# Optimization experiments

Measured on AMD Instinct MI355X. Metric: run time of the kernel, lower is better.

## Reference

```python
import jax, jax.numpy as jnp
import numpy as np

SIZE_IN = 1024
SIZE_OUT = 1024
N_ROWS = 16384
MAX_VAL = 127.0  # nemo=False -> int8 path


def _quantize(t, max_val):
    """Per-tensor symmetric quantization matching the torch code.
    scale = max_val / max(|min(t)|, |max(t)|) (1.0 if t_max==0);
    q = clamp(round(scale*t), -max_val, max_val) cast to int8."""
    t_max = jnp.maximum(jnp.abs(jnp.min(t)), jnp.abs(jnp.max(t)))
    t_max = jnp.where(t_max == 0.0, 1.0, t_max)
    scale = max_val / t_max
    q = jnp.clip(jnp.round(scale * t), -max_val, max_val).astype(jnp.int8)
    return q, scale


def setup_inputs() -> dict:
    key = jax.random.key(0)
    kx, kw, kb = jax.random.split(key, 3)
    x = jax.random.normal(kx, (N_ROWS, SIZE_IN), dtype=jnp.float32)
    # kaiming_uniform_(a=sqrt(5)) -> uniform(-1/sqrt(fan_in), 1/sqrt(fan_in))
    bound = 1.0 / np.sqrt(SIZE_IN)
    weight = jax.random.uniform(kw, (SIZE_OUT, SIZE_IN), dtype=jnp.float32,
                                minval=-bound, maxval=bound)
    bias = jax.random.uniform(kb, (SIZE_OUT,), dtype=jnp.float32,
                              minval=-bound, maxval=bound)
    return {"x": x, "weight": weight, "bias": bias}


def reference(x, weight, bias):
    qw, sw = _quantize(weight, MAX_VAL)          # [SIZE_OUT, SIZE_IN] int8
    qx, sa = _quantize(x, MAX_VAL)               # [N, SIZE_IN] int8
    qb, sb = _quantize(bias, MAX_VAL)            # [SIZE_OUT] int8
    # for the approximate axx kernel), then dequantize.
    acc = jnp.matmul(qx.astype(jnp.int32), qw.astype(jnp.int32).T)  # [N, SIZE_OUT]
    out = acc.astype(jnp.float32) / (sa * sw)
    out = out + qb.astype(jnp.float32) / sb
    return out
```

## Files before the change

### kernel.cpp

```cpp
#include <hip/hip_runtime.h>


#define M_ROWS 16384
#define K_DIM  1024
#define N_OUT  1024

typedef int v4i __attribute__((ext_vector_type(4)));

__device__ __forceinline__ void gload_lds16(const void* g, void* l) {
  __builtin_amdgcn_global_load_lds(
      (const __attribute__((address_space(1))) void*)g,
      (__attribute__((address_space(3))) void*)l, 16, 0, 0);
}

__device__ __forceinline__ float block_reduce_max4(float m, float* red) {
#pragma unroll
  for (int off = 32; off > 0; off >>= 1)
    m = fmaxf(m, __shfl_down(m, off));
  const int wid = threadIdx.x >> 6, lane = threadIdx.x & 63;
  if (lane == 0) red[wid] = m;
  __syncthreads();
  float r = fmaxf(fmaxf(red[0], red[1]), fmaxf(red[2], red[3]));
  __syncthreads();
  return r;
}

__global__ void amax_stage1(const float* __restrict__ src, int n4,
                            float* __restrict__ partials) {
  __shared__ float red[4];
  float m = 0.0f;
  const int stride = gridDim.x * blockDim.x;
  for (int idx = blockIdx.x * blockDim.x + threadIdx.x; idx < n4; idx += stride) {
    float4 v = ((const float4*)src)[idx];
    m = fmaxf(m, fmaxf(fmaxf(fabsf(v.x), fabsf(v.y)), fmaxf(fabsf(v.z), fabsf(v.w))));
  }
  float r = block_reduce_max4(m, red);
  if (threadIdx.x == 0) partials[blockIdx.x] = r;
}

__global__ void finalize_kernel(const float* __restrict__ px, int npx,
                                const float* __restrict__ pw, int npw,
                                const float* __restrict__ bias,
                                float* __restrict__ amax,
                                float* __restrict__ bdeq) {
  __shared__ float red[4];
  const int tid = threadIdx.x;

  float m = 0.0f;
  for (int i = tid; i < npx; i += 256) m = fmaxf(m, px[i]);
  float rx = block_reduce_max4(m, red);

  m = 0.0f;
  for (int i = tid; i < npw; i += 256) m = fmaxf(m, pw[i]);
  float rw = block_reduce_max4(m, red);

  float4 bv = ((const float4*)bias)[tid];
  m = fmaxf(fmaxf(fabsf(bv.x), fabsf(bv.y)), fmaxf(fabsf(bv.z), fabsf(bv.w)));
  float rb = block_reduce_max4(m, red);

  if (rx == 0.0f) rx = 1.0f;
  if (rw == 0.0f) rw = 1.0f;
  if (rb == 0.0f) rb = 1.0f;
  if (tid == 0) {
    amax[0] = rx;
    amax[1] = rw;
    amax[2] = rb;
  }
  const float sb = 127.0f / rb;
  float4 q;
  q.x = fminf(fmaxf(rintf(sb * bv.x), -127.0f), 127.0f) / sb;
  q.y = fminf(fmaxf(rintf(sb * bv.y), -127.0f), 127.0f) / sb;
  q.z = fminf(fmaxf(rintf(sb * bv.z), -127.0f), 127.0f) / sb;
  q.w = fminf(fmaxf(rintf(sb * bv.w), -127.0f), 127.0f) / sb;
  ((float4*)bdeq)[tid] = q;
}

__global__ void quant_kernel(const float* __restrict__ src, signed char* __restrict__ dst,
                             int n4, const float* __restrict__ amax, int slot) {
  const float s = 127.0f / amax[slot];
  const int stride = gridDim.x * blockDim.x;
  for (int idx = blockIdx.x * blockDim.x + threadIdx.x; idx < n4; idx += stride) {
    float4 v = ((const float4*)src)[idx];
    int q0 = (int)fminf(fmaxf(rintf(s * v.x), -127.0f), 127.0f);
    int q1 = (int)fminf(fmaxf(rintf(s * v.y), -127.0f), 127.0f);
    int q2 = (int)fminf(fmaxf(rintf(s * v.z), -127.0f), 127.0f);
    int q3 = (int)fminf(fmaxf(rintf(s * v.w), -127.0f), 127.0f);
    unsigned int packed = (q0 & 0xff) | ((q1 & 0xff) << 8) |
                          ((q2 & 0xff) << 16) | ((q3 & 0xff) << 24);
    ((unsigned int*)dst)[idx] = packed;
  }
}


__global__ __launch_bounds__(512, 2) void gemm_kernel(
    const signed char* __restrict__ qx, const signed char* __restrict__ qw,
    const float* __restrict__ amax, const float* __restrict__ bdeq,
    float* __restrict__ out) {
  __shared__ char lds[131072];

  const int tid  = threadIdx.x;
  const int w    = tid >> 6;
  const int lane = tid & 63;
  const int wm = w >> 2;
  const int wn = w & 3;
  const int fr = lane & 15;
  const int q  = lane >> 4;

  const int bid = blockIdx.x;
  const int wg  = (bid & 7) * 32 + (bid >> 3);
  const int Mbase = (wg >> 2) * 256;
  const int Nbase = (wg & 3) * 256;

  const signed char* gA = qx + (size_t)Mbase * K_DIM;
  const signed char* gB = qw + (size_t)Nbase * K_DIM;

  const int lrow = lane >> 3;
  const int lcol = ((lane & 7) ^ lrow) << 4;

  const int u0    = (q ^ (fr & 7)) << 4;
  const int aoffA = (wm * 64 + fr) * 128 + u0;
  const int aoffB = (wn * 32 + fr) * 128 + u0;

  v4i acc[8][4] = {};
  v4i Ar[4][2];
  v4i Br[2][2][2];

#define STG(MAT, BUF, HALF, T)                                                 \
  do {                                                                         \
    const signed char* _gb = (MAT) ? gB : gA;                                  \
    char* _l = lds + ((MAT) ? 65536 : 0) + (BUF)*32768 + (HALF)*16384 +        \
               w * 2048;                                                       \
    size_t _ro = (size_t)((HALF)*128 + w * 16 + lrow) * K_DIM + (T)*128 + lcol;\
    gload_lds16(_gb + _ro, _l);                                                \
    gload_lds16(_gb + _ro + (size_t)8 * K_DIM, _l + 1024);                     \
  } while (0)

#define RD_A(BUF, MH)                                                          \
  do {                                                                         \
    const char* _A = lds + (BUF)*32768 + (MH)*16384;                           \
    _Pragma("unroll") for (int f = 0; f < 4; ++f) {                            \
      Ar[f][0] = *(const v4i*)(_A + (aoffA + f * 2048));                       \
      Ar[f][1] = *(const v4i*)(_A + ((aoffA ^ 64) + f * 2048));                \
    }                                                                          \
  } while (0)

#define RD_B(BUF, NH)                                                          \
  do {                                                                         \
    const char* _B = lds + 65536 + (BUF)*32768 + (NH)*16384;                   \
    _Pragma("unroll") for (int g = 0; g < 2; ++g) {                            \
      Br[NH][g][0] = *(const v4i*)(_B + (aoffB + g * 2048));                   \
      Br[NH][g][1] = *(const v4i*)(_B + ((aoffB ^ 64) + g * 2048));            \
    }                                                                          \
  } while (0)

#define MM(MH, NH)                                                             \
  do {                                                                         \
    __builtin_amdgcn_s_barrier();                                              \
    asm volatile("s_waitcnt lgkmcnt(0)" ::: "memory");                         \
    __builtin_amdgcn_sched_barrier(0);                                         \
    __builtin_amdgcn_s_setprio(1);                                             \
    _Pragma("unroll") for (int kk = 0; kk < 2; ++kk)                           \
      _Pragma("unroll") for (int f = 0; f < 4; ++f)                            \
        _Pragma("unroll") for (int g = 0; g < 2; ++g)                          \
          acc[(MH)*4 + f][(NH)*2 + g] = __builtin_amdgcn_mfma_i32_16x16x64_i8( \
              Ar[f][kk], Br[NH][g][kk], acc[(MH)*4 + f][(NH)*2 + g], 0, 0, 0); \
    __builtin_amdgcn_s_setprio(0);                                             \
  } while (0)

#define VM(N) asm volatile("s_waitcnt vmcnt(" #N ")" ::: "memory")
#define BAR() __builtin_amdgcn_s_barrier()

  STG(0, 0, 0, 0); STG(1, 0, 0, 0); STG(1, 0, 1, 0); STG(0, 0, 1, 0);
  STG(0, 1, 0, 1); STG(1, 1, 0, 1); STG(1, 1, 1, 1); STG(0, 1, 1, 1);
  VM(8);
  BAR();

  for (int j = 0; j < 4; ++j) {
    const int t2 = (2 * j + 2) & 7;
    const int t3 = (2 * j + 3) & 7;
    RD_A(0, 0); RD_B(0, 0);                    MM(0, 0);        BAR();
    RD_B(0, 1); STG(0, 0, 0, t2);              MM(0, 1);        BAR();
    RD_A(0, 1); STG(1, 0, 0, t2);              MM(1, 1);        BAR();
    STG(1, 0, 1, t2);                          MM(1, 0); VM(6); BAR();
    RD_A(1, 0); RD_B(1, 0); STG(0, 0, 1, t2);  MM(0, 0);        BAR();
    RD_B(1, 1); STG(0, 1, 0, t3); STG(1, 1, 0, t3); MM(0, 1);   BAR();
    RD_A(1, 1); STG(1, 1, 1, t3);              MM(1, 1);        BAR();
    STG(0, 1, 1, t3);                          MM(1, 0); VM(8); BAR();
  }
#undef MM
#undef RD_A
#undef RD_B
#undef STG
#undef VM
#undef BAR

  const float inv_denom = (amax[0] * amax[1]) * (1.0f / 16129.0f);
#pragma unroll
  for (int f = 0; f < 8; ++f) {
    const int row0 = Mbase + wm * 64 + (f & 3) * 16 + (f >> 2) * 128 + q * 4;
#pragma unroll
    for (int g = 0; g < 4; ++g) {
      const int col = Nbase + wn * 32 + (g & 1) * 16 + (g >> 1) * 128 + fr;
      const float bb = bdeq[col];
#pragma unroll
      for (int i = 0; i < 4; ++i) {
        out[(size_t)(row0 + i) * N_OUT + col] = (float)acc[f][g][i] * inv_denom + bb;
      }
    }
  }
}

extern "C" void kernel_launch(void* const* d_in, const int* in_sizes, int n_in,
                              void* d_out, int out_size, void* d_ws, size_t ws_size,
                              hipStream_t stream) {
  const float* x = (const float*)d_in[0];
  const float* w = (const float*)d_in[1];
  const float* b = (const float*)d_in[2];
  float* out = (float*)d_out;

  char* ws = (char*)d_ws;
  float* amax = (float*)ws;
  float* bdeq = (float*)(ws + 256);
  float* px   = (float*)(ws + 8192);
  float* pw   = (float*)(ws + 16384 + 8192);
  signed char* qw = (signed char*)(ws + 65536);
  signed char* qx = (signed char*)(ws + (1 << 21));

  const int NPX = 2048, NPW = 256;
  hipLaunchKernelGGL(amax_stage1, dim3(NPX), dim3(256), 0, stream, x, M_ROWS * K_DIM / 4, px);
  hipLaunchKernelGGL(amax_stage1, dim3(NPW), dim3(256), 0, stream, w, N_OUT * K_DIM / 4, pw);
  hipLaunchKernelGGL(finalize_kernel, dim3(1), dim3(256), 0, stream, px, NPX, pw, NPW, b, amax, bdeq);
  hipLaunchKernelGGL(quant_kernel, dim3(2048), dim3(256), 0, stream, x, qx, M_ROWS * K_DIM / 4, amax, 0);
  hipLaunchKernelGGL(quant_kernel, dim3(256), dim3(256), 0, stream, w, qw, N_OUT * K_DIM / 4, amax, 1);
  hipLaunchKernelGGL(gemm_kernel, dim3(64 * 4), dim3(512), 0, stream, qx, qw, amax, bdeq, out);
}
```

Before: 65.62 us.

## Peel last K iteration, interleave epilogue stores with final MFMAs, drop extra barrier

```diff
diff --git a/kernel.cpp b/kernel.cpp
--- a/kernel.cpp
+++ b/kernel.cpp
@@ -121,6 +121,8 @@
   const int aoffA = (wm * 64 + fr) * 128 + u0;
   const int aoffB = (wn * 32 + fr) * 128 + u0;
 
+  const float inv_denom = (amax[0] * amax[1]) * (1.0f / 16129.0f);
+
   v4i acc[8][4] = {};
   v4i Ar[4][2];
   v4i Br[2][2][2];
@@ -153,61 +155,70 @@
     }                                                                          \
   } while (0)
 
-#define MM(MH, NH)                                                             \
-  do {                                                                         \
-    __builtin_amdgcn_s_barrier();                                              \
-    asm volatile("s_waitcnt lgkmcnt(0)" ::: "memory");                         \
-    __builtin_amdgcn_sched_barrier(0);                                         \
-    __builtin_amdgcn_s_setprio(1);                                             \
+#define MFMA_Q(MH, NH)                                                         \
+  do {                                                                         \
     _Pragma("unroll") for (int kk = 0; kk < 2; ++kk)                           \
       _Pragma("unroll") for (int f = 0; f < 4; ++f)                            \
         _Pragma("unroll") for (int g = 0; g < 2; ++g)                          \
           acc[(MH)*4 + f][(NH)*2 + g] = __builtin_amdgcn_mfma_i32_16x16x64_i8( \
               Ar[f][kk], Br[NH][g][kk], acc[(MH)*4 + f][(NH)*2 + g], 0, 0, 0); \
-    __builtin_amdgcn_s_setprio(0);                                             \
+  } while (0)
+
+#define STORE_Q(MH, NH)                                                        \
+  do {                                                                         \
+    _Pragma("unroll") for (int f = 0; f < 4; ++f) {                            \
+      const int _row0 = Mbase + wm * 64 + f * 16 + (MH)*128 + q * 4;           \
+      _Pragma("unroll") for (int g = 0; g < 2; ++g) {                          \
+        const int _col = Nbase + wn * 32 + g * 16 + (NH)*128 + fr;             \
+        const float _bb = bdeq[_col];                                          \
+        _Pragma("unroll") for (int i = 0; i < 4; ++i)                          \
+          out[(size_t)(_row0 + i) * N_OUT + _col] =                            \
+              (float)acc[(MH)*4 + f][(NH)*2 + g][i] * inv_denom + _bb;         \
+      }                                                                        \
+    }                                                                          \
   } while (0)
 
 #define VM(N) asm volatile("s_waitcnt vmcnt(" #N ")" ::: "memory")
-#define BAR() __builtin_amdgcn_s_barrier()
+#define ENDPH()                                                                \
+  do {                                                                         \
+    asm volatile("s_waitcnt lgkmcnt(0)" ::: "memory");                         \
+    __builtin_amdgcn_s_barrier();                                              \
+  } while (0)
 
   STG(0, 0, 0, 0); STG(1, 0, 0, 0); STG(1, 0, 1, 0); STG(0, 0, 1, 0);
   STG(0, 1, 0, 1); STG(1, 1, 0, 1); STG(1, 1, 1, 1); STG(0, 1, 1, 1);
   VM(8);
-  BAR();
-
-  for (int j = 0; j < 4; ++j) {
-    const int t2 = (2 * j + 2) & 7;
-    const int t3 = (2 * j + 3) & 7;
-    RD_A(0, 0); RD_B(0, 0);                    MM(0, 0);        BAR();
-    RD_B(0, 1); STG(0, 0, 0, t2);              MM(0, 1);        BAR();
-    RD_A(0, 1); STG(1, 0, 0, t2);              MM(1, 1);        BAR();
-    STG(1, 0, 1, t2);                          MM(1, 0); VM(6); BAR();
-    RD_A(1, 0); RD_B(1, 0); STG(0, 0, 1, t2);  MM(0, 0);        BAR();
-    RD_B(1, 1); STG(0, 1, 0, t3); STG(1, 1, 0, t3); MM(0, 1);   BAR();
-    RD_A(1, 1); STG(1, 1, 1, t3);              MM(1, 1);        BAR();
-    STG(0, 1, 1, t3);                          MM(1, 0); VM(8); BAR();
-  }
-#undef MM
+  __builtin_amdgcn_s_barrier();
+
+  for (int j = 0; j < 3; ++j) {
+    const int t2 = 2 * j + 2;
+    const int t3 = 2 * j + 3;
+    RD_A(0, 0); RD_B(0, 0);                    MFMA_Q(0, 0);        ENDPH();
+    STG(0, 0, 0, t2); RD_B(0, 1);              MFMA_Q(0, 1);        ENDPH();
+    STG(1, 0, 0, t2); RD_A(0, 1);              MFMA_Q(1, 1);        ENDPH();
+    STG(1, 0, 1, t2);                          MFMA_Q(1, 0); VM(6); ENDPH();
+    STG(0, 0, 1, t2); RD_A(1, 0); RD_B(1, 0);  MFMA_Q(0, 0);        ENDPH();
+    STG(0, 1, 0, t3); STG(1, 1, 0, t3); RD_B(1, 1); MFMA_Q(0, 1);   ENDPH();
+    STG(1, 1, 1, t3); RD_A(1, 1);              MFMA_Q(1, 1);        ENDPH();
+    STG(0, 1, 1, t3);                          MFMA_Q(1, 0); VM(8); ENDPH();
+  }
+
+  RD_A(0, 0); RD_B(0, 0);  MFMA_Q(0, 0);        ENDPH();
+  RD_B(0, 1);              MFMA_Q(0, 1);        ENDPH();
+  RD_A(0, 1);              MFMA_Q(1, 1);        ENDPH();
+                           MFMA_Q(1, 0); VM(0); ENDPH();
+  RD_A(1, 0); RD_B(1, 0);  MFMA_Q(0, 0);  STORE_Q(0, 0);
+  RD_B(1, 1);              MFMA_Q(0, 1);  STORE_Q(0, 1);
+  RD_A(1, 1);              MFMA_Q(1, 1);  STORE_Q(1, 1);
+                           MFMA_Q(1, 0);  STORE_Q(1, 0);
+
+#undef STG
 #undef RD_A
 #undef RD_B
-#undef STG
+#undef MFMA_Q
+#undef STORE_Q
 #undef VM
-#undef BAR
-
-  const float inv_denom = (amax[0] * amax[1]) * (1.0f / 16129.0f);
-#pragma unroll
-  for (int f = 0; f < 8; ++f) {
-    const int row0 = Mbase + wm * 64 + (f & 3) * 16 + (f >> 2) * 128 + q * 4;
-#pragma unroll
-    for (int g = 0; g < 4; ++g) {
-      const int col = Nbase + wn * 32 + (g & 1) * 16 + (g >> 1) * 128 + fr;
-      const float bb = bdeq[col];
-#pragma unroll
-      for (int i = 0; i < 4; ++i) {
-        out[(size_t)(row0 + i) * N_OUT + col] = (float)acc[f][g][i] * inv_denom + bb;
-      }
-    }
-  }
+#undef ENDPH
 }
 
 extern "C" void kernel_launch(void* const* d_in, const int* in_sizes, int n_in,
```

Result: faster. 63.20 us (-3.7%).
